# Performance work log

Measured on AMD Instinct MI355X. Metric: run time of the kernel, lower is better.

Reference implementation:

```python
import jax, jax.numpy as jnp
import numpy as np

T, B, L, CTX, H = 512, 512, 16, 64, 128
STATE_DIM, SHOT, PID, DATA = 32, 12, 35, 23


def setup_inputs() -> dict:
    key = jax.random.key(0)
    ks = jax.random.split(key, 64)
    k = iter(ks)
    def rn(shape, s=0.1):
        return (jax.random.normal(next(k), shape) * s).astype(jnp.float32)
    xs = jax.random.normal(next(k), (T, B, DATA), jnp.float32)
    xs = xs.at[:, :, 12].set(jax.random.randint(next(k), (T, B), 0, SHOT).astype(jnp.float32))
    xs = xs.at[:, :, 17].set(jax.random.randint(next(k), (T, B), 0, PID).astype(jnp.float32))
    xs = xs.at[:, :, 20].set(jax.random.randint(next(k), (T, B), 0, SHOT).astype(jnp.float32))
    return dict(
        total_xs=jnp.zeros((1,), jnp.float32),
        xs=xs,
        ts=jnp.linspace(0.0, 2.0, T).astype(jnp.float32),
        noise_std=jnp.asarray(0.1, jnp.float32),
        z0_noise=jax.random.normal(next(k), (B, L), jnp.float32),
        bm_noise=jax.random.normal(next(k), (T - 1, B, L), jnp.float32),
        shot_emb=rn((SHOT, 8)), player_emb=rn((PID, 8)),
        gru_wih=rn((3 * H, STATE_DIM)), gru_whh=rn((3 * H, H)),
        gru_bih=rn((3 * H,)), gru_bhh=rn((3 * H,)),
        enc_w=rn((CTX, H)), enc_b=rn((CTX,)),
        qz0_w=rn((2 * L, CTX)), qz0_b=rn((2 * L,)),
        f_w1=rn((H, L + CTX)), f_b1=rn((H,)), f_w2=rn((H, H)), f_b2=rn((H,)),
        f_w3=rn((L, H)), f_b3=rn((L,)),
        h_w1=rn((H, L)), h_b1=rn((H,)), h_w2=rn((H, H)), h_b2=rn((H,)),
        h_w3=rn((L, H)), h_b3=rn((L,)),
        g_w1=rn((L, H)), g_b1=rn((L, H)), g_w2=rn((L, H)), g_b2=rn((L,)),
        proj_w=rn((STATE_DIM, L)), proj_b=rn((STATE_DIM,)),
        pz0_mean=jnp.zeros((1, L), jnp.float32), pz0_logstd=jnp.zeros((1, L), jnp.float32),
        act_w=rn((128, L)), act_b=rn((128,)),
        act_land_w=rn((2, 128)), act_shot_w=rn((SHOT, 128)), act_move_w=rn((2, 128)),
    )


def _forward(xs, noise_std, shot_emb, player_emb, gru_wih, gru_whh, gru_bih, gru_bhh,
             enc_w, enc_b, qz0_w, qz0_b,
             f_w1, f_b1, f_w2, f_b2, f_w3, f_b3,
             h_w1, h_b1, h_w2, h_b2, h_w3, h_b3,
             g_w1, g_b1, g_w2, g_b2,
             proj_w, proj_b, pz0_mean, pz0_logstd,
             act_w, act_b, act_land_w, act_shot_w, act_move_w,
             ts, z0_noise, bm_noise):
    # --- SDE_embed_and_transform: replace shot/player id cols with embeddings ---
    state = xs[:, :, :18]
    shot_ids = state[:, :, 12].astype(jnp.int32)
    pid_ids = state[:, :, 17].astype(jnp.int32)
    state_t = jnp.concatenate([state[:, :, :12], shot_emb[shot_ids],
                               state[:, :, 13:17], player_emb[pid_ids]], axis=-1)  # (T,B,32)
    xs_t = jnp.concatenate([state_t, xs[:, :, 18:]], axis=-1)  # (T,B,37)
    # --- Encoder: GRU over time-reversed states, linear head, flip back ---
    def gru_step(h, xt):
        gi = xt @ gru_wih.T + gru_bih
        gh = h @ gru_whh.T + gru_bhh
        ir, iz, inn = jnp.split(gi, 3, axis=-1)
        hr, hz, hn = jnp.split(gh, 3, axis=-1)
        r = jax.nn.sigmoid(ir + hr)
        zg = jax.nn.sigmoid(iz + hz)
        n = jnp.tanh(inn + r * hn)
        hnew = (1.0 - zg) * n + zg * h
        return hnew, hnew
    h0 = jnp.zeros((xs.shape[1], gru_whh.shape[1]), xs.dtype)
    _, hs = jax.lax.scan(gru_step, h0, state_t[::-1])
    ctx = (hs @ enc_w.T + enc_b)[::-1]  # (T,B,CTX)
    # --- posterior z0 ---
    qm, qls = jnp.split(ctx[0] @ qz0_w.T + qz0_b, 2, axis=1)
    z0 = qm + jnp.exp(qls) * z0_noise
    # --- Euler-Maruyama with logqp; searchsorted(right) -> ctx[min(i+1,T-1)] = ctx[i+1] ---
    dts = ts[1:] - ts[:-1]  # (T-1,)
    dW = jnp.sqrt(dts)[:, None, None] * bm_noise
    ctx_steps = ctx[1:]
    def mlp3(x, w1, b1, w2, b2, w3, b3):
        h1 = jax.nn.softplus(x @ w1.T + b1)
        h2 = jax.nn.softplus(h1 @ w2.T + b2)
        return h2 @ w3.T + b3
    def g_diag(y):  # (B,L): per-latent-dim scalar nets, batched over L
        hg = jax.nn.softplus(y[:, :, None] * g_w1[None] + g_b1[None])  # (B,L,H)
        return jax.nn.sigmoid(jnp.einsum('blh,lh->bl', hg, g_w2) + g_b2)
    def sde_step(z, inp):
        c, dw, dt = inp
        f_val = mlp3(jnp.concatenate([z, c], axis=1), f_w1, f_b1, f_w2, f_b2, f_w3, f_b3)
        h_val = mlp3(z, h_w1, h_b1, h_w2, h_b2, h_w3, h_b3)
        g_val = g_diag(z)
        u = (f_val - h_val) / g_val
        logr = 0.5 * jnp.sum(u * u, axis=1) * dt
        z_new = z + f_val * dt + g_val * dw
        return z_new, (z_new, logr)
    _, (z_tail, log_ratio) = jax.lax.scan(sde_step, z0, (ctx_steps, dW, dts))
    zs = jnp.concatenate([z0[None], z_tail], axis=0)  # (T,B,L)
    _xs = zs @ proj_w.T + proj_b  # (T,B,32)
    # --- action model losses ---
    a = jax.nn.relu(zs @ act_w.T + act_b)
    land = (a @ act_land_w.T).reshape(-1, 2)
    shot_logits = (a @ act_shot_w.T).reshape(-1, act_shot_w.shape[0])
    move = (a @ act_move_w.T).reshape(-1, 2)
    true_actions = xs_t[:, :, -5:]
    true_land = true_actions[:, :, :2].reshape(-1, 2)
    true_move = true_actions[:, :, 3:].reshape(-1, 2)
    true_shot = true_actions[:, :, 2].astype(jnp.int32).reshape(-1)
    land_loss = jnp.mean((land - true_land) ** 2)
    move_loss = jnp.mean((move - true_move) ** 2)
    logp = jax.nn.log_softmax(shot_logits, axis=-1)
    picked = jnp.take_along_axis(logp, true_shot[:, None], axis=1)[:, 0]
    mask = (true_shot != 0).astype(logp.dtype)  # CrossEntropy ignore_index=0
    shot_loss = -jnp.sum(picked * mask) / jnp.maximum(jnp.sum(mask), 1.0)
    # --- reconstruction log-likelihood ---
    xs_state = xs_t[:, :, :STATE_DIM]
    LOG2PI = 1.8378770664093453
    log_pxs = jnp.mean(jnp.sum(
        -0.5 * ((xs_state - _xs) / noise_std) ** 2 - jnp.log(noise_std) - 0.5 * LOG2PI,
        axis=(0, 2)))
    # --- KL(q(z0) || p(z0)) ---
    var_q = jnp.exp(2.0 * qls)
    var_p = jnp.exp(2.0 * pz0_logstd)
    kl = pz0_logstd - qls + (var_q + (qm - pz0_mean) ** 2) / (2.0 * var_p) - 0.5
    logqp0 = jnp.mean(jnp.sum(kl, axis=1))
    logqp_path = jnp.mean(jnp.sum(log_ratio, axis=0))
    return log_pxs, logqp0 + logqp_path + land_loss + shot_loss + move_loss


def reference(total_xs, xs, ts, noise_std, z0_noise, bm_noise, shot_emb, player_emb,
              gru_wih, gru_whh, gru_bih, gru_bhh, enc_w, enc_b, qz0_w, qz0_b,
              f_w1, f_b1, f_w2, f_b2, f_w3, f_b3, h_w1, h_b1, h_w2, h_b2, h_w3, h_b3,
              g_w1, g_b1, g_w2, g_b2, proj_w, proj_b, pz0_mean, pz0_logstd,
              act_w, act_b, act_land_w, act_shot_w, act_move_w):
    return _forward(xs, noise_std, shot_emb, player_emb, gru_wih, gru_whh, gru_bih, gru_bhh,
                    enc_w, enc_b, qz0_w, qz0_b,
                    f_w1, f_b1, f_w2, f_b2, f_w3, f_b3,
                    h_w1, h_b1, h_w2, h_b2, h_w3, h_b3,
                    g_w1, g_b1, g_w2, g_b2,
                    proj_w, proj_b, pz0_mean, pz0_logstd,
                    act_w, act_b, act_land_w, act_shot_w, act_move_w,
                    ts, z0_noise, bm_noise)
```

## Files before the change

### kernel.cpp

```cpp
#include <hip/hip_runtime.h>
#include <cstdint>

typedef _Float16 f16;
typedef _Float16 f16x2 __attribute__((ext_vector_type(2)));

#define T_STEPS 512
#define B_SZ 512
#define LOG2PI 1.8378770664093453f

__device__ __forceinline__ uint32_t packh2(float a, float b) {
  f16x2 v; v[0] = (f16)a; v[1] = (f16)b;
  return __builtin_bit_cast(uint32_t, v);
}

__device__ __forceinline__ float fdot2(uint32_t a, uint32_t b, float c) {
#if defined(__AMDGCN__) && __has_builtin(__builtin_amdgcn_fdot2)
  return __builtin_amdgcn_fdot2(__builtin_bit_cast(f16x2, a),
                                __builtin_bit_cast(f16x2, b), c, false);
#else
  f16x2 x = __builtin_bit_cast(f16x2, a), y = __builtin_bit_cast(f16x2, b);
  return c + (float)x[0] * (float)y[0] + (float)x[1] * (float)y[1];
#endif
}

#define DOT4(acc, w0, w1, w2, w3, v)                                     \
  do {                                                                   \
    acc = fdot2((w0), (v).x, acc); acc = fdot2((w1), (v).y, acc);        \
    acc = fdot2((w2), (v).z, acc); acc = fdot2((w3), (v).w, acc);        \
  } while (0)

__device__ __forceinline__ float sigmoidf_(float x) {
  return 1.0f / (1.0f + __expf(-x));
}
__device__ __forceinline__ float tanhf_(float x) {
  float ax = fabsf(x);
  float t = __expf(-2.0f * ax);
  float r = (1.0f - t) / (1.0f + t);
  return copysignf(r, x);
}
__device__ __forceinline__ float softplusf_(float x) {
  return fmaxf(x, 0.0f) + __logf(1.0f + __expf(-fabsf(x)));
}

__global__ __launch_bounds__(256) void k_embed(
    const float* __restrict__ xs, const float* __restrict__ shot_emb,
    const float* __restrict__ player_emb, f16* __restrict__ state_t,
    float* __restrict__ accums) {
  if (blockIdx.x == 0 && threadIdx.x < 16) accums[threadIdx.x] = 0.0f;
  size_t idx = (size_t)blockIdx.x * 256 + threadIdx.x;
  const float* xp = xs + idx * 23;
  f16* op = state_t + idx * 32;
  int sid = (int)xp[12];
  int pid = (int)xp[17];
#pragma unroll
  for (int i = 0; i < 12; ++i) op[i] = (f16)xp[i];
  const float* se = shot_emb + sid * 8;
#pragma unroll
  for (int i = 0; i < 8; ++i) op[12 + i] = (f16)se[i];
#pragma unroll
  for (int i = 0; i < 4; ++i) op[20 + i] = (f16)xp[13 + i];
  const float* pe = player_emb + pid * 8;
#pragma unroll
  for (int i = 0; i < 8; ++i) op[24 + i] = (f16)pe[i];
}

__global__ __launch_bounds__(448, 4) void k_gru(
    const f16* __restrict__ state_t, const float* __restrict__ wih,
    const float* __restrict__ whh, const float* __restrict__ bih,
    const float* __restrict__ bhh, const float* __restrict__ enc_w,
    const float* __restrict__ enc_b, const float* __restrict__ qz0_w,
    const float* __restrict__ qz0_b, const float* __restrict__ z0_noise,
    const float* __restrict__ pz0_mean, const float* __restrict__ pz0_logstd,
    f16* __restrict__ ctx, float* __restrict__ z0_out,
    float* __restrict__ accums) {
  __shared__ __align__(16) uint32_t s_x[16];
  __shared__ __align__(16) uint32_t s_h[64];
  __shared__ float s_gi[384], s_gh[384];
  __shared__ float s_ctx0[64];
  __shared__ float s_q[32];

  const int tid = threadIdx.x;
  const int bg = blockIdx.x;
  const uint32_t* stu = (const uint32_t*)state_t;

  uint32_t wA[64];
  uint32_t wB[16];
  float bi = 0.f, bh = 0.f, encbr = 0.f;

  if (tid < 384) {
    const float* whr = whh + (size_t)tid * 128;
#pragma unroll
    for (int i = 0; i < 64; ++i) wA[i] = packh2(whr[2 * i], whr[2 * i + 1]);
    const float* wxr = wih + (size_t)tid * 32;
#pragma unroll
    for (int i = 0; i < 16; ++i) wB[i] = packh2(wxr[2 * i], wxr[2 * i + 1]);
    bi = bih[tid];
    bh = bhh[tid];
  } else {
    int cc = tid - 384;
    const float* wer = enc_w + (size_t)cc * 128;
#pragma unroll
    for (int i = 0; i < 64; ++i) wA[i] = packh2(wer[2 * i], wer[2 * i + 1]);
    encbr = enc_b[cc];
  }

  if (tid < 64) s_h[tid] = 0u;
  if (tid < 4)
    *(uint4*)&s_x[tid * 4] =
        *(const uint4*)(stu + ((size_t)(T_STEPS - 1) * B_SZ + bg) * 16 + tid * 4);
  float h_old = 0.0f;
  __syncthreads();

  for (int t = T_STEPS - 1; t >= 0; --t) {
    uint4 xpref = make_uint4(0, 0, 0, 0);
    if (tid >= 128 && tid < 132 && t > 0)
      xpref = *(const uint4*)(stu + ((size_t)(t - 1) * B_SZ + bg) * 16 +
                              (tid - 128) * 4);
    if (tid < 384) {
      float ax0 = bi, ax1 = 0.f;
      const uint4* xq = (const uint4*)s_x;
#pragma unroll
      for (int j = 0; j < 4; ++j) {
        uint4 v = xq[j];
        if (j & 1) { DOT4(ax1, wB[4 * j], wB[4 * j + 1], wB[4 * j + 2], wB[4 * j + 3], v); }
        else       { DOT4(ax0, wB[4 * j], wB[4 * j + 1], wB[4 * j + 2], wB[4 * j + 3], v); }
      }
      float ah0 = bh, ah1 = 0.f;
      const uint4* hq = (const uint4*)s_h;
#pragma unroll
      for (int j = 0; j < 16; ++j) {
        uint4 v = hq[j];
        if (j & 1) { DOT4(ah1, wA[4 * j], wA[4 * j + 1], wA[4 * j + 2], wA[4 * j + 3], v); }
        else       { DOT4(ah0, wA[4 * j], wA[4 * j + 1], wA[4 * j + 2], wA[4 * j + 3], v); }
      }
      s_gi[tid] = ax0 + ax1;
      s_gh[tid] = ah0 + ah1;
    } else if (t < T_STEPS - 1) {
      int cc = tid - 384;
      float a0 = encbr, a1 = 0.f;
      const uint4* hq = (const uint4*)s_h;
#pragma unroll
      for (int j = 0; j < 16; ++j) {
        uint4 v = hq[j];
        if (j & 1) { DOT4(a1, wA[4 * j], wA[4 * j + 1], wA[4 * j + 2], wA[4 * j + 3], v); }
        else       { DOT4(a0, wA[4 * j], wA[4 * j + 1], wA[4 * j + 2], wA[4 * j + 3], v); }
      }
      ctx[((size_t)(t + 1) * B_SZ + bg) * 64 + cc] = (f16)(a0 + a1);
    }
    __syncthreads();
    if (tid < 128) {
      float r = sigmoidf_(s_gi[tid] + s_gh[tid]);
      float zg = sigmoidf_(s_gi[128 + tid] + s_gh[128 + tid]);
      float n = tanhf_(s_gi[256 + tid] + r * s_gh[256 + tid]);
      float hnew = (1.0f - zg) * n + zg * h_old;
      h_old = hnew;
      ((f16*)s_h)[tid] = (f16)hnew;
    } else if (tid >= 128 && tid < 132 && t > 0) {
      *(uint4*)&s_x[(tid - 128) * 4] = xpref;
    }
    __syncthreads();
  }

  if (tid >= 384) {
    int cc = tid - 384;
    float a0 = encbr, a1 = 0.f;
    const uint4* hq = (const uint4*)s_h;
#pragma unroll
    for (int j = 0; j < 16; ++j) {
      uint4 v = hq[j];
      if (j & 1) { DOT4(a1, wA[4 * j], wA[4 * j + 1], wA[4 * j + 2], wA[4 * j + 3], v); }
      else       { DOT4(a0, wA[4 * j], wA[4 * j + 1], wA[4 * j + 2], wA[4 * j + 3], v); }
    }
    float val = a0 + a1;
    ctx[(size_t)bg * 64 + cc] = (f16)val;
    s_ctx0[cc] = val;
  }
  __syncthreads();
  if (tid < 32) {
    float acc = qz0_b[tid];
#pragma unroll 8
    for (int k = 0; k < 64; ++k) acc += qz0_w[tid * 64 + k] * s_ctx0[k];
    s_q[tid] = acc;
  }
  __syncthreads();
  if (tid < 16) {
    float qm = s_q[tid], qls = s_q[16 + tid];
    float z0v = qm + __expf(qls) * z0_noise[bg * 16 + tid];
    z0_out[bg * 16 + tid] = z0v;
    float pm = pz0_mean[tid], pls = pz0_logstd[tid];
    float var_q = __expf(2.0f * qls);
    float var_p = __expf(2.0f * pls);
    float dm = qm - pm;
    float kl = pls - qls + (var_q + dm * dm) / (2.0f * var_p) - 0.5f;
    atomicAdd(&accums[5], kl);
  }
}

__global__ __launch_bounds__(256, 2) void k_sde(
    const f16* __restrict__ ctx, const float* __restrict__ z0_in,
    const float* __restrict__ ts, const float* __restrict__ bm_noise,
    const float* __restrict__ fw1, const float* __restrict__ fb1,
    const float* __restrict__ fw2, const float* __restrict__ fb2,
    const float* __restrict__ fw3, const float* __restrict__ fb3,
    const float* __restrict__ hw1, const float* __restrict__ hb1,
    const float* __restrict__ hw2, const float* __restrict__ hb2,
    const float* __restrict__ hw3, const float* __restrict__ hb3,
    const float* __restrict__ gw1, const float* __restrict__ gb1,
    const float* __restrict__ gw2, const float* __restrict__ gb2,
    f16* __restrict__ zs, float* __restrict__ accums) {
  __shared__ __align__(16) uint32_t s_x2[40];
  __shared__ __align__(16) uint32_t s_h1f[64];
  __shared__ __align__(16) uint32_t s_h1h[64];
  __shared__ __align__(16) uint32_t s_h2[2][64];
  __shared__ float s_zf[16];
  __shared__ __align__(16) float s_gp[128];
  __shared__ __align__(16) float s_p3[256];
  __shared__ float s_dts[T_STEPS];

  const int tid = threadIdx.x;
  const int bg = blockIdx.x;

  uint32_t uw[56];
  uint32_t wP2[64];
  uint32_t wP3[8];
  float bias1r = 0.f, bias2r = 0.f, gb2r = 0.f, fb3r = 0.f, hb3r = 0.f;

  if (tid < 128) {
    const float* w = fw1 + (size_t)tid * 80;
#pragma unroll
    for (int i = 0; i < 40; ++i) uw[i] = packh2(w[2 * i], w[2 * i + 1]);
    bias1r = fb1[tid];
  } else {
    int u = tid - 128;
    const float* w = hw1 + (size_t)u * 16;
#pragma unroll
    for (int i = 0; i < 8; ++i) uw[i] = packh2(w[2 * i], w[2 * i + 1]);
    bias1r = hb1[u];
    int l = u & 15, k8 = u >> 4;
#pragma unroll
    for (int i = 0; i < 16; ++i) {
      int h = k8 * 16 + i;
      uw[8 + i] = __builtin_bit_cast(uint32_t, gw1[l * 128 + h]);
      uw[24 + i] = __builtin_bit_cast(uint32_t, gb1[l * 128 + h]);
      uw[40 + i] = __builtin_bit_cast(uint32_t, gw2[l * 128 + h]);
    }
  }
  {
    int mlp = tid >> 7, u = tid & 127;
    const float* w = (mlp ? hw2 : fw2) + (size_t)u * 128;
#pragma unroll
    for (int i = 0; i < 64; ++i) wP2[i] = packh2(w[2 * i], w[2 * i + 1]);
    bias2r = (mlp ? hb2 : fb2)[u];
  }
  {
    int mlp = tid >> 7, o = tid & 15, k8 = (tid >> 4) & 7;
    const float* w = (mlp ? hw3 : fw3) + (size_t)o * 128 + k8 * 16;
#pragma unroll
    for (int i = 0; i < 8; ++i) wP3[i] = packh2(w[2 * i], w[2 * i + 1]);
  }
  if (tid < 16) {
    fb3r = fb3[tid];
    hb3r = hb3[tid];
    gb2r = gb2[tid];
  }
  for (int i = tid; i < T_STEPS - 1; i += 256) s_dts[i] = ts[i + 1] - ts[i];

  if (tid < 16) {
    float z = z0_in[bg * 16 + tid];
    s_zf[tid] = z;
    ((f16*)s_x2)[tid] = (f16)z;
    zs[(size_t)bg * 16 + tid] = (f16)z;
  }
  if (tid >= 16 && tid < 24) {
    int q = tid - 16;
    *(uint4*)&s_x2[8 + q * 4] =
        *(const uint4*)((const uint32_t*)ctx + ((size_t)1 * B_SZ + bg) * 32 + q * 4);
  }
  float path_acc = 0.0f;
  __syncthreads();

  for (int t = 0; t < T_STEPS - 1; ++t) {
    float bm_cur = 0.f;
    uint4 cpref = make_uint4(0, 0, 0, 0);
    if (tid < 16) bm_cur = bm_noise[((size_t)t * B_SZ + bg) * 16 + tid];
    if (tid >= 16 && tid < 24 && t <= T_STEPS - 3) {
      int q = tid - 16;
      cpref = *(const uint4*)((const uint32_t*)ctx +
                              ((size_t)(t + 2) * B_SZ + bg) * 32 + q * 4);
    }
    if (tid < 128) {
      float a0 = bias1r, a1 = 0.f;
      const uint4* xq = (const uint4*)s_x2;
#pragma unroll
      for (int j = 0; j < 10; ++j) {
        uint4 v = xq[j];
        if (j & 1) { DOT4(a1, uw[4 * j], uw[4 * j + 1], uw[4 * j + 2], uw[4 * j + 3], v); }
        else       { DOT4(a0, uw[4 * j], uw[4 * j + 1], uw[4 * j + 2], uw[4 * j + 3], v); }
      }
      ((f16*)s_h1f)[tid] = (f16)softplusf_(a0 + a1);
    } else {
      int u = tid - 128;
      const uint4* zq = (const uint4*)s_x2;
      float a0 = bias1r, a1 = 0.f;
      uint4 v0 = zq[0], v1 = zq[1];
      DOT4(a0, uw[0], uw[1], uw[2], uw[3], v0);
      DOT4(a1, uw[4], uw[5], uw[6], uw[7], v1);
      ((f16*)s_h1h)[u] = (f16)softplusf_(a0 + a1);
      int l = u & 15, k8 = u >> 4;
      float y = s_zf[l];
      float acc = 0.f;
#pragma unroll
      for (int i = 0; i < 16; ++i) {
        float pre = fmaf(y, __builtin_bit_cast(float, uw[8 + i]),
                         __builtin_bit_cast(float, uw[24 + i]));
        acc = fmaf(softplusf_(pre), __builtin_bit_cast(float, uw[40 + i]), acc);
      }
      s_gp[l * 8 + k8] = acc;
    }
    __syncthreads();
    {
      const uint4* hq = (const uint4*)((tid >> 7) ? s_h1h : s_h1f);
      float a0 = bias2r, a1 = 0.f, a2 = 0.f, a3 = 0.f;
#pragma unroll
      for (int j = 0; j < 16; j += 4) {
        uint4 v0 = hq[j], v1 = hq[j + 1], v2 = hq[j + 2], v3 = hq[j + 3];
        DOT4(a0, wP2[4 * j], wP2[4 * j + 1], wP2[4 * j + 2], wP2[4 * j + 3], v0);
        DOT4(a1, wP2[4 * j + 4], wP2[4 * j + 5], wP2[4 * j + 6], wP2[4 * j + 7], v1);
        DOT4(a2, wP2[4 * j + 8], wP2[4 * j + 9], wP2[4 * j + 10], wP2[4 * j + 11], v2);
        DOT4(a3, wP2[4 * j + 12], wP2[4 * j + 13], wP2[4 * j + 14], wP2[4 * j + 15], v3);
      }
      ((f16*)s_h2[tid >> 7])[tid & 127] = (f16)softplusf_((a0 + a1) + (a2 + a3));
    }
    __syncthreads();
    {
      int mlp = tid >> 7, o = tid & 15, k8 = (tid >> 4) & 7;
      const uint4* hq = (const uint4*)&s_h2[mlp][k8 * 8];
      uint4 v0 = hq[0], v1 = hq[1];
      float a0 = 0.f, a1 = 0.f;
      DOT4(a0, wP3[0], wP3[1], wP3[2], wP3[3], v0);
      DOT4(a1, wP3[4], wP3[5], wP3[6], wP3[7], v1);
      s_p3[(mlp * 16 + o) * 8 + k8] = a0 + a1;
    }
    __syncthreads();
    if (tid < 16) {
      int l = tid;
      const float4* fp = (const float4*)&s_p3[l * 8];
      const float4* hp = (const float4*)&s_p3[(16 + l) * 8];
      const float4* gp = (const float4*)&s_gp[l * 8];
      float4 f0 = fp[0], f1v = fp[1], h0 = hp[0], h1v = hp[1];
      float4 g0 = gp[0], g1 = gp[1];
      float fv = fb3r + ((f0.x + f0.y) + (f0.z + f0.w)) +
                 ((f1v.x + f1v.y) + (f1v.z + f1v.w));
      float hv = hb3r + ((h0.x + h0.y) + (h0.z + h0.w)) +
                 ((h1v.x + h1v.y) + (h1v.z + h1v.w));
      float gv = sigmoidf_(gb2r + ((g0.x + g0.y) + (g0.z + g0.w)) +
                           ((g1.x + g1.y) + (g1.z + g1.w)));
      float dt = s_dts[t];
      float u = (fv - hv) / gv;
      float lsum = u * u;
      lsum += __shfl_xor(lsum, 1);
      lsum += __shfl_xor(lsum, 2);
      lsum += __shfl_xor(lsum, 4);
      lsum += __shfl_xor(lsum, 8);
      if (l == 0) path_acc += 0.5f * lsum * dt;
      float zn = s_zf[l] + fv * dt + gv * (sqrtf(dt) * bm_cur);
      s_zf[l] = zn;
      ((f16*)s_x2)[l] = (f16)zn;
      zs[((size_t)(t + 1) * B_SZ + bg) * 16 + l] = (f16)zn;
    } else if (tid >= 16 && tid < 24 && t <= T_STEPS - 3) {
      int q = tid - 16;
      *(uint4*)&s_x2[8 + q * 4] = cpref;
    }
    __syncthreads();
  }
  if (tid == 0) atomicAdd(&accums[6], path_acc);
}

__global__ __launch_bounds__(256) void k_dec(
    const f16* __restrict__ zs, const f16* __restrict__ state_t,
    const float* __restrict__ xs, const float* __restrict__ proj_w,
    const float* __restrict__ proj_b, const float* __restrict__ act_w,
    const float* __restrict__ act_b, const float* __restrict__ land_w,
    const float* __restrict__ shot_w, const float* __restrict__ move_w,
    float* __restrict__ accums) {
  __shared__ __align__(16) uint32_t s_proj[32 * 8];
  __shared__ __align__(16) uint32_t s_act[128 * 8];
  __shared__ __align__(16) uint32_t s_head[128 * 8];
  __shared__ float s_pb[32], s_ab[128];
  __shared__ float s_red[4 * 5];

  const int tid = threadIdx.x;
  if (tid < 256) {
    int i = tid >> 3, kp = tid & 7;
    s_proj[tid] = packh2(proj_w[i * 16 + 2 * kp], proj_w[i * 16 + 2 * kp + 1]);
  }
  for (int id = tid; id < 1024; id += 256) {
    int j = id >> 3, kp = id & 7;
    s_act[id] = packh2(act_w[j * 16 + 2 * kp], act_w[j * 16 + 2 * kp + 1]);
  }
  for (int id = tid; id < 1024; id += 256) {
    int j = id >> 3, p = id & 7;
    int h0 = 2 * p, h1 = 2 * p + 1;
    float w0 = (h0 < 2) ? land_w[h0 * 128 + j]
                        : (h0 < 14 ? shot_w[(h0 - 2) * 128 + j]
                                   : move_w[(h0 - 14) * 128 + j]);
    float w1 = (h1 < 2) ? land_w[h1 * 128 + j]
                        : (h1 < 14 ? shot_w[(h1 - 2) * 128 + j]
                                   : move_w[(h1 - 14) * 128 + j]);
    s_head[j * 8 + p] = packh2(w0, w1);
  }
  if (tid < 32) s_pb[tid] = proj_b[tid];
  if (tid < 128) s_ab[tid] = act_b[tid];
  __syncthreads();

  size_t idx0 = (size_t)blockIdx.x * 512 + tid;
  size_t idx1 = idx0 + 256;
  uint32_t zA[8], zB[8];
  {
    const uint4* za = (const uint4*)(zs + idx0 * 16);
    const uint4* zb = (const uint4*)(zs + idx1 * 16);
    uint4 a0 = za[0], a1 = za[1], b0 = zb[0], b1 = zb[1];
    zA[0] = a0.x; zA[1] = a0.y; zA[2] = a0.z; zA[3] = a0.w;
    zA[4] = a1.x; zA[5] = a1.y; zA[6] = a1.z; zA[7] = a1.w;
    zB[0] = b0.x; zB[1] = b0.y; zB[2] = b0.z; zB[3] = b0.w;
    zB[4] = b1.x; zB[5] = b1.y; zB[6] = b1.z; zB[7] = b1.w;
  }
  uint32_t stA[16], stB[16];
  {
// ... 118 lines not shown

extern "C" void kernel_launch(void* const* d_in, const int* in_sizes, int n_in,
                              void* d_out, int out_size, void* d_ws,
                              size_t ws_size, hipStream_t stream) {
  const float* xs = (const float*)d_in[1];
  const float* ts = (const float*)d_in[2];
  const float* noise_std = (const float*)d_in[3];
  const float* z0_noise = (const float*)d_in[4];
  const float* bm_noise = (const float*)d_in[5];
  const float* shot_emb = (const float*)d_in[6];
  const float* player_emb = (const float*)d_in[7];
  const float* gru_wih = (const float*)d_in[8];
  const float* gru_whh = (const float*)d_in[9];
  const float* gru_bih = (const float*)d_in[10];
  const float* gru_bhh = (const float*)d_in[11];
  const float* enc_w = (const float*)d_in[12];
  const float* enc_b = (const float*)d_in[13];
  const float* qz0_w = (const float*)d_in[14];
  const float* qz0_b = (const float*)d_in[15];
  const float* f_w1 = (const float*)d_in[16];
  const float* f_b1 = (const float*)d_in[17];
  const float* f_w2 = (const float*)d_in[18];
  const float* f_b2 = (const float*)d_in[19];
  const float* f_w3 = (const float*)d_in[20];
  const float* f_b3 = (const float*)d_in[21];
  const float* h_w1 = (const float*)d_in[22];
  const float* h_b1 = (const float*)d_in[23];
  const float* h_w2 = (const float*)d_in[24];
  const float* h_b2 = (const float*)d_in[25];
  const float* h_w3 = (const float*)d_in[26];
  const float* h_b3 = (const float*)d_in[27];
  const float* g_w1 = (const float*)d_in[28];
  const float* g_b1 = (const float*)d_in[29];
  const float* g_w2 = (const float*)d_in[30];
  const float* g_b2 = (const float*)d_in[31];
  const float* proj_w = (const float*)d_in[32];
  const float* proj_b = (const float*)d_in[33];
  const float* pz0_mean = (const float*)d_in[34];
  const float* pz0_logstd = (const float*)d_in[35];
  const float* act_w = (const float*)d_in[36];
  const float* act_b = (const float*)d_in[37];
  const float* act_land_w = (const float*)d_in[38];
  const float* act_shot_w = (const float*)d_in[39];
  const float* act_move_w = (const float*)d_in[40];

  char* ws = (char*)d_ws;
  float* accums = (float*)ws;
  f16* state_t = (f16*)(ws + 256);
  f16* ctx = (f16*)(ws + 256 + 16777216);
  float* z0b = (float*)(ws + 256 + 16777216 + 33554432);
  f16* zs = (f16*)(ws + 256 + 16777216 + 33554432 + 32768);

  k_embed<<<1024, 256, 0, stream>>>(xs, shot_emb, player_emb, state_t, accums);
  k_gru<<<512, 448, 0, stream>>>(state_t, gru_wih, gru_whh, gru_bih, gru_bhh,
                                 enc_w, enc_b, qz0_w, qz0_b, z0_noise, pz0_mean,
                                 pz0_logstd, ctx, z0b, accums);
  k_sde<<<512, 256, 0, stream>>>(ctx, z0b, ts, bm_noise, f_w1, f_b1, f_w2, f_b2,
                                 f_w3, f_b3, h_w1, h_b1, h_w2, h_b2, h_w3, h_b3,
                                 g_w1, g_b1, g_w2, g_b2, zs, accums);
  k_dec<<<512, 256, 0, stream>>>(zs, state_t, xs, proj_w, proj_b, act_w, act_b,
                                 act_land_w, act_shot_w, act_move_w, accums);
  k_fin<<<1, 64, 0, stream>>>(accums, noise_std, (float*)d_out);
}
```

Before: 2.005 ms.

## Repartition GRU and SDE recurrences so each thread computes two rows

The GRU kernel moves from 448 to 256 threads per block. Each thread now holds two gate rows and folds bih+bhh for the r/z gates, which drops one barrier-separated stage and lets the loop read x directly. Encoder context outputs are staged in a 64-row shared ring buffer and written to global memory in coalesced bursts. The SDE kernel is repartitioned the same way: two rows per thread, the final layer is reduced with shuffles instead of an extra shared-memory stage, and zs is buffered in shared memory and written once at the end. The intent is fewer barriers and less per-step global traffic, in exchange for much higher register pressure per thread and less thread-level parallelism per step.

```diff
diff --git a/kernel.cpp b/kernel.cpp
--- a/kernel.cpp
+++ b/kernel.cpp
@@ -64,7 +64,7 @@
   for (int i = 0; i < 8; ++i) op[24 + i] = (f16)pe[i];
 }
 
-__global__ __launch_bounds__(448, 4) void k_gru(
+__global__ __launch_bounds__(256, 2) void k_gru(
     const f16* __restrict__ state_t, const float* __restrict__ wih,
     const float* __restrict__ whh, const float* __restrict__ bih,
     const float* __restrict__ bhh, const float* __restrict__ enc_w,
@@ -73,9 +73,10 @@
     const float* __restrict__ pz0_mean, const float* __restrict__ pz0_logstd,
     f16* __restrict__ ctx, float* __restrict__ z0_out,
     float* __restrict__ accums) {
-  __shared__ __align__(16) uint32_t s_x[16];
   __shared__ __align__(16) uint32_t s_h[64];
-  __shared__ float s_gi[384], s_gh[384];
+  __shared__ __align__(16) float s_grz[128][2];
+  __shared__ __align__(16) float s_gn[128][2];
+  __shared__ __align__(16) f16 s_cbuf[64][64];
   __shared__ float s_ctx0[64];
   __shared__ float s_q[32];
 
@@ -83,100 +84,176 @@
   const int bg = blockIdx.x;
   const uint32_t* stu = (const uint32_t*)state_t;
 
-  uint32_t wA[64];
-  uint32_t wB[16];
-  float bi = 0.f, bh = 0.f, encbr = 0.f;
-
-  if (tid < 384) {
-    const float* whr = whh + (size_t)tid * 128;
-#pragma unroll
-    for (int i = 0; i < 64; ++i) wA[i] = packh2(whr[2 * i], whr[2 * i + 1]);
-    const float* wxr = wih + (size_t)tid * 32;
-#pragma unroll
-    for (int i = 0; i < 16; ++i) wB[i] = packh2(wxr[2 * i], wxr[2 * i + 1]);
-    bi = bih[tid];
-    bh = bhh[tid];
+  uint32_t wh0[64], wh1[64], wx0[16], wx1[16];
+  float b0 = 0.f, b1 = 0.f, b0h = 0.f, b1h = 0.f, encbr = 0.f;
+
+  if (tid < 128) {
+    const float* r0 = whh + (size_t)tid * 128;
+    const float* r1 = whh + (size_t)(128 + tid) * 128;
+#pragma unroll
+    for (int i = 0; i < 64; ++i) {
+      wh0[i] = packh2(r0[2 * i], r0[2 * i + 1]);
+      wh1[i] = packh2(r1[2 * i], r1[2 * i + 1]);
+    }
+    const float* x0 = wih + (size_t)tid * 32;
+    const float* x1 = wih + (size_t)(128 + tid) * 32;
+#pragma unroll
+    for (int i = 0; i < 16; ++i) {
+      wx0[i] = packh2(x0[2 * i], x0[2 * i + 1]);
+      wx1[i] = packh2(x1[2 * i], x1[2 * i + 1]);
+    }
+    b0 = bih[tid] + bhh[tid];
+    b1 = bih[128 + tid] + bhh[128 + tid];
+  } else if (tid < 192) {
+    int u = tid - 128;
+    const float* r0 = whh + (size_t)(256 + 2 * u) * 128;
+    const float* r1 = whh + (size_t)(256 + 2 * u + 1) * 128;
+#pragma unroll
+    for (int i = 0; i < 64; ++i) {
+      wh0[i] = packh2(r0[2 * i], r0[2 * i + 1]);
+      wh1[i] = packh2(r1[2 * i], r1[2 * i + 1]);
+    }
+    const float* x0 = wih + (size_t)(256 + 2 * u) * 32;
+    const float* x1 = wih + (size_t)(256 + 2 * u + 1) * 32;
+#pragma unroll
+    for (int i = 0; i < 16; ++i) {
+      wx0[i] = packh2(x0[2 * i], x0[2 * i + 1]);
+      wx1[i] = packh2(x1[2 * i], x1[2 * i + 1]);
+    }
+    b0 = bih[256 + 2 * u];
+    b0h = bhh[256 + 2 * u];
+    b1 = bih[256 + 2 * u + 1];
+    b1h = bhh[256 + 2 * u + 1];
   } else {
-    int cc = tid - 384;
-    const float* wer = enc_w + (size_t)cc * 128;
-#pragma unroll
-    for (int i = 0; i < 64; ++i) wA[i] = packh2(wer[2 * i], wer[2 * i + 1]);
-    encbr = enc_b[cc];
+    int c = tid - 192;
+    const float* er = enc_w + (size_t)c * 128;
+#pragma unroll
+    for (int i = 0; i < 64; ++i) wh0[i] = packh2(er[2 * i], er[2 * i + 1]);
+    encbr = enc_b[c];
   }
 
   if (tid < 64) s_h[tid] = 0u;
-  if (tid < 4)
-    *(uint4*)&s_x[tid * 4] =
-        *(const uint4*)(stu + ((size_t)(T_STEPS - 1) * B_SZ + bg) * 16 + tid * 4);
   float h_old = 0.0f;
   __syncthreads();
 
   for (int t = T_STEPS - 1; t >= 0; --t) {
-    uint4 xpref = make_uint4(0, 0, 0, 0);
-    if (tid >= 128 && tid < 132 && t > 0)
-      xpref = *(const uint4*)(stu + ((size_t)(t - 1) * B_SZ + bg) * 16 +
-                              (tid - 128) * 4);
-    if (tid < 384) {
-      float ax0 = bi, ax1 = 0.f;
-      const uint4* xq = (const uint4*)s_x;
-#pragma unroll
-      for (int j = 0; j < 4; ++j) {
-        uint4 v = xq[j];
-        if (j & 1) { DOT4(ax1, wB[4 * j], wB[4 * j + 1], wB[4 * j + 2], wB[4 * j + 3], v); }
-        else       { DOT4(ax0, wB[4 * j], wB[4 * j + 1], wB[4 * j + 2], wB[4 * j + 3], v); }
-      }
-      float ah0 = bh, ah1 = 0.f;
+    const uint4* xr = (const uint4*)(stu + ((size_t)t * B_SZ + bg) * 16);
+    uint4 xv0 = xr[0], xv1 = xr[1], xv2 = xr[2], xv3 = xr[3];
+    if (tid < 128) {
+      float aR = b0, aRb = 0.f, aZ = b1, aZb = 0.f;
+      DOT4(aR, wx0[0], wx0[1], wx0[2], wx0[3], xv0);
+      DOT4(aRb, wx0[4], wx0[5], wx0[6], wx0[7], xv1);
+      DOT4(aR, wx0[8], wx0[9], wx0[10], wx0[11], xv2);
+      DOT4(aRb, wx0[12], wx0[13], wx0[14], wx0[15], xv3);
+      DOT4(aZ, wx1[0], wx1[1], wx1[2], wx1[3], xv0);
+      DOT4(aZb, wx1[4], wx1[5], wx1[6], wx1[7], xv1);
+      DOT4(aZ, wx1[8], wx1[9], wx1[10], wx1[11], xv2);
+      DOT4(aZb, wx1[12], wx1[13], wx1[14], wx1[15], xv3);
       const uint4* hq = (const uint4*)s_h;
 #pragma unroll
       for (int j = 0; j < 16; ++j) {
         uint4 v = hq[j];
-        if (j & 1) { DOT4(ah1, wA[4 * j], wA[4 * j + 1], wA[4 * j + 2], wA[4 * j + 3], v); }
-        else       { DOT4(ah0, wA[4 * j], wA[4 * j + 1], wA[4 * j + 2], wA[4 * j + 3], v); }
+        if (j & 1) {
+          DOT4(aRb, wh0[4 * j], wh0[4 * j + 1], wh0[4 * j + 2], wh0[4 * j + 3], v);
+          DOT4(aZb, wh1[4 * j], wh1[4 * j + 1], wh1[4 * j + 2], wh1[4 * j + 3], v);
+        } else {
+          DOT4(aR, wh0[4 * j], wh0[4 * j + 1], wh0[4 * j + 2], wh0[4 * j + 3], v);
+          DOT4(aZ, wh1[4 * j], wh1[4 * j + 1], wh1[4 * j + 2], wh1[4 * j + 3], v);
+        }
       }
-      s_gi[tid] = ax0 + ax1;
-      s_gh[tid] = ah0 + ah1;
-    } else if (t < T_STEPS - 1) {
-      int cc = tid - 384;
-      float a0 = encbr, a1 = 0.f;
+      *(float2*)&s_grz[tid][0] = make_float2(aR + aRb, aZ + aZb);
+    } else if (tid < 192) {
+      int u = tid - 128;
+      float aI0 = b0, aI0b = 0.f, aI1 = b1, aI1b = 0.f;
+      DOT4(aI0, wx0[0], wx0[1], wx0[2], wx0[3], xv0);
+      DOT4(aI0b, wx0[4], wx0[5], wx0[6], wx0[7], xv1);
+      DOT4(aI0, wx0[8], wx0[9], wx0[10], wx0[11], xv2);
+      DOT4(aI0b, wx0[12], wx0[13], wx0[14], wx0[15], xv3);
+      DOT4(aI1, wx1[0], wx1[1], wx1[2], wx1[3], xv0);
+      DOT4(aI1b, wx1[4], wx1[5], wx1[6], wx1[7], xv1);
+      DOT4(aI1, wx1[8], wx1[9], wx1[10], wx1[11], xv2);
+      DOT4(aI1b, wx1[12], wx1[13], wx1[14], wx1[15], xv3);
+      float aH0 = b0h, aH0b = 0.f, aH1 = b1h, aH1b = 0.f;
       const uint4* hq = (const uint4*)s_h;
 #pragma unroll
       for (int j = 0; j < 16; ++j) {
         uint4 v = hq[j];
-        if (j & 1) { DOT4(a1, wA[4 * j], wA[4 * j + 1], wA[4 * j + 2], wA[4 * j + 3], v); }
-        else       { DOT4(a0, wA[4 * j], wA[4 * j + 1], wA[4 * j + 2], wA[4 * j + 3], v); }
+        if (j & 1) {
+          DOT4(aH0b, wh0[4 * j], wh0[4 * j + 1], wh0[4 * j + 2], wh0[4 * j + 3], v);
+          DOT4(aH1b, wh1[4 * j], wh1[4 * j + 1], wh1[4 * j + 2], wh1[4 * j + 3], v);
+        } else {
+          DOT4(aH0, wh0[4 * j], wh0[4 * j + 1], wh0[4 * j + 2], wh0[4 * j + 3], v);
+          DOT4(aH1, wh1[4 * j], wh1[4 * j + 1], wh1[4 * j + 2], wh1[4 * j + 3], v);
+        }
       }
-      ctx[((size_t)(t + 1) * B_SZ + bg) * 64 + cc] = (f16)(a0 + a1);
+      *(float4*)&s_gn[2 * u][0] =
+          make_float4(aI0 + aI0b, aH0 + aH0b, aI1 + aI1b, aH1 + aH1b);
+    } else if (t < T_STEPS - 1) {
+      int c = tid - 192;
+      float e0 = encbr, e1 = 0.f;
+      const uint4* hq = (const uint4*)s_h;
+#pragma unroll
+      for (int j = 0; j < 16; ++j) {
+        uint4 v = hq[j];
+        if (j & 1) {
+          DOT4(e1, wh0[4 * j], wh0[4 * j + 1], wh0[4 * j + 2], wh0[4 * j + 3], v);
+        } else {
+          DOT4(e0, wh0[4 * j], wh0[4 * j + 1], wh0[4 * j + 2], wh0[4 * j + 3], v);
+        }
+      }
+      s_cbuf[(t + 1) & 63][c] = (f16)(e0 + e1);
     }
     __syncthreads();
     if (tid < 128) {
-      float r = sigmoidf_(s_gi[tid] + s_gh[tid]);
-      float zg = sigmoidf_(s_gi[128 + tid] + s_gh[128 + tid]);
-      float n = tanhf_(s_gi[256 + tid] + r * s_gh[256 + tid]);
+      float2 rz = *(const float2*)&s_grz[tid][0];
+      float2 nn = *(const float2*)&s_gn[tid][0];
+      float r = sigmoidf_(rz.x);
+      float zg = sigmoidf_(rz.y);
+      float n = tanhf_(nn.x + r * nn.y);
       float hnew = (1.0f - zg) * n + zg * h_old;
       h_old = hnew;
       ((f16*)s_h)[tid] = (f16)hnew;
-    } else if (tid >= 128 && tid < 132 && t > 0) {
-      *(uint4*)&s_x[(tid - 128) * 4] = xpref;
+    } else if (tid >= 192 && (t & 63) == 63) {
+      int lane = tid & 63;
+      int seg = lane & 7;
+#pragma unroll
+      for (int it = 0; it < 8; ++it) {
+        int row = (t + 1) + it * 8 + (lane >> 3);
+        uint4 v = *(const uint4*)((const uint32_t*)&s_cbuf[row & 63][0] + seg * 4);
+        *(uint4*)((uint32_t*)ctx + ((size_t)row * B_SZ + bg) * 32 + seg * 4) = v;
+      }
     }
     __syncthreads();
   }
 
-  if (tid >= 384) {
-    int cc = tid - 384;
-    float a0 = encbr, a1 = 0.f;
+  if (tid >= 192) {
+    int c = tid - 192;
+    float e0 = encbr, e1 = 0.f;
     const uint4* hq = (const uint4*)s_h;
 #pragma unroll
     for (int j = 0; j < 16; ++j) {
       uint4 v = hq[j];
-      if (j & 1) { DOT4(a1, wA[4 * j], wA[4 * j + 1], wA[4 * j + 2], wA[4 * j + 3], v); }
-      else       { DOT4(a0, wA[4 * j], wA[4 * j + 1], wA[4 * j + 2], wA[4 * j + 3], v); }
-    }
-    float val = a0 + a1;
-    ctx[(size_t)bg * 64 + cc] = (f16)val;
-    s_ctx0[cc] = val;
+      if (j & 1) {
+        DOT4(e1, wh0[4 * j], wh0[4 * j + 1], wh0[4 * j + 2], wh0[4 * j + 3], v);
+      } else {
+        DOT4(e0, wh0[4 * j], wh0[4 * j + 1], wh0[4 * j + 2], wh0[4 * j + 3], v);
+      }
+    }
+    float val = e0 + e1;
+    s_ctx0[c] = val;
+    s_cbuf[0][c] = (f16)val;
   }
   __syncthreads();
-  if (tid < 32) {
+  if (tid >= 192) {
+    int lane = tid & 63;
+    int seg = lane & 7;
+#pragma unroll
+    for (int it = 0; it < 8; ++it) {
+      int row = it * 8 + (lane >> 3);
+      uint4 v = *(const uint4*)((const uint32_t*)&s_cbuf[row][0] + seg * 4);
+      *(uint4*)((uint32_t*)ctx + ((size_t)row * B_SZ + bg) * 32 + seg * 4) = v;
+    }
+  } else if (tid < 32) {
     float acc = qz0_b[tid];
 #pragma unroll 8
     for (int k = 0; k < 64; ++k) acc += qz0_w[tid * 64 + k] * s_ctx0[k];
@@ -208,172 +285,254 @@
     const float* __restrict__ gw1, const float* __restrict__ gb1,
     const float* __restrict__ gw2, const float* __restrict__ gb2,
     f16* __restrict__ zs, float* __restrict__ accums) {
-  __shared__ __align__(16) uint32_t s_x2[40];
+  __shared__ __align__(16) uint32_t s_x2z[8];
+  __shared__ float s_zf[16];
   __shared__ __align__(16) uint32_t s_h1f[64];
   __shared__ __align__(16) uint32_t s_h1h[64];
   __shared__ __align__(16) uint32_t s_h2[2][64];
-  __shared__ float s_zf[16];
-  __shared__ __align__(16) float s_gp[128];
-  __shared__ __align__(16) float s_p3[256];
+  __shared__ float s_gpw[2][16];
+  __shared__ __align__(16) float s_v3[32];
   __shared__ float s_dts[T_STEPS];
+  __shared__ __align__(16) f16 s_zbuf[T_STEPS * 16];
 
   const int tid = threadIdx.x;
   const int bg = blockIdx.x;
 
-  uint32_t uw[56];
-  uint32_t wP2[64];
-  uint32_t wP3[8];
-  float bias1r = 0.f, bias2r = 0.f, gb2r = 0.f, fb3r = 0.f, hb3r = 0.f;
-
-  if (tid < 128) {
-    const float* w = fw1 + (size_t)tid * 80;
-#pragma unroll
-    for (int i = 0; i < 40; ++i) uw[i] = packh2(w[2 * i], w[2 * i + 1]);
-    bias1r = fb1[tid];
+  uint32_t wa[80];
+  uint32_t wb[32];
+  float gw1v[16], gb1v[16], gw2v[16];
+  float ba = 0.f, bb = 0.f, fb3r = 0.f, hb3r = 0.f, gb2r = 0.f;
+
+  if (tid < 64) {
+    const float* r0 = fw1 + (size_t)(2 * tid) * 80;
+    const float* r1 = fw1 + (size_t)(2 * tid + 1) * 80;
+#pragma unroll
+    for (int i = 0; i < 40; ++i) {
+      wa[i] = packh2(r0[2 * i], r0[2 * i + 1]);
+      wa[40 + i] = packh2(r1[2 * i], r1[2 * i + 1]);
+    }
+    ba = fb1[2 * tid];
+    bb = fb1[2 * tid + 1];
+    int k8 = tid >> 3, mlp = (tid >> 2) & 1, o4 = tid & 3;
+    const float* w3src = mlp ? hw3 : fw3;
+#pragma unroll
+    for (int oo = 0; oo < 4; ++oo)
+#pragma unroll
+      for (int j = 0; j < 8; ++j)
+        wb[oo * 8 + j] = packh2(w3src[(o4 * 4 + oo) * 128 + k8 * 16 + 2 * j],
+                                w3src[(o4 * 4 + oo) * 128 + k8 * 16 + 2 * j + 1]);
+    if (tid < 16) {
+      fb3r = fb3[tid];
+      hb3r = hb3[tid];
+      gb2r = gb2[tid];
+    }
+  } else if (tid < 128) {
+    int u = tid - 64;
+    const float* r0 = fw2 + (size_t)(2 * u) * 128;
+    const float* r1 = fw2 + (size_t)(2 * u + 1) * 128;
+#pragma unroll
+    for (int i = 0; i < 64; ++i) {
+      wa[i] = packh2(r0[2 * i], r0[2 * i + 1]);
+      wb[i & 15] = wb[i & 15];
+    }
+    ba = fb2[2 * u];
+    bb = fb2[2 * u + 1];
+    int l = u & 15, c4 = u >> 4;
+#pragma unroll
+    for (int j = 0; j < 16; ++j) {
+      int h = c4 * 16 + j;
+      gw1v[j] = gw1[l * 128 + h];
+      gb1v[j] = gb1[l * 128 + h];
+      gw2v[j] = gw2[l * 128 + h];
+    }
+  } else if (tid < 192) {
+    int u = tid - 128;
+    const float* r0 = hw2 + (size_t)(2 * u) * 128;
+#pragma unroll
+    for (int i = 0; i < 64; ++i) wa[i] = packh2(r0[2 * i], r0[2 * i + 1]);
+    const float* z0r = hw1 + (size_t)(2 * u) * 16;
+    const float* z1r = hw1 + (size_t)(2 * u + 1) * 16;
+#pragma unroll
+    for (int i = 0; i < 8; ++i) {
+      wb[i] = packh2(z0r[2 * i], z0r[2 * i + 1]);
+      wb[8 + i] = packh2(z1r[2 * i], z1r[2 * i + 1]);
+    }
+    ba = hb2[2 * u];
+    bb = hb2[2 * u + 1];
   } else {
+    int i2 = tid - 192;
+    int l = i2 & 15, c4 = i2 >> 4;
+#pragma unroll
+    for (int j = 0; j < 16; ++j) {
+      int h = 64 + c4 * 16 + j;
+      gw1v[j] = gw1[l * 128 + h];
+      gb1v[j] = gb1[l * 128 + h];
+      gw2v[j] = gw2[l * 128 + h];
+    }
+  }
+  uint32_t wc[64];
+  if (tid >= 64 && tid < 128) {
+    int u = tid - 64;
+    const float* r1 = fw2 + (size_t)(2 * u + 1) * 128;
+#pragma unroll
+    for (int i = 0; i < 64; ++i) wc[i] = packh2(r1[2 * i], r1[2 * i + 1]);
+  } else if (tid >= 128 && tid < 192) {
     int u = tid - 128;
-    const float* w = hw1 + (size_t)u * 16;
-#pragma unroll
-    for (int i = 0; i < 8; ++i) uw[i] = packh2(w[2 * i], w[2 * i + 1]);
-    bias1r = hb1[u];
-    int l = u & 15, k8 = u >> 4;
-#pragma unroll
-    for (int i = 0; i < 16; ++i) {
-      int h = k8 * 16 + i;
-      uw[8 + i] = __builtin_bit_cast(uint32_t, gw1[l * 128 + h]);
-      uw[24 + i] = __builtin_bit_cast(uint32_t, gb1[l * 128 + h]);
-      uw[40 + i] = __builtin_bit_cast(uint32_t, gw2[l * 128 + h]);
-    }
-  }
-  {
-    int mlp = tid >> 7, u = tid & 127;
-    const float* w = (mlp ? hw2 : fw2) + (size_t)u * 128;
-#pragma unroll
-    for (int i = 0; i < 64; ++i) wP2[i] = packh2(w[2 * i], w[2 * i + 1]);
-    bias2r = (mlp ? hb2 : fb2)[u];
-  }
-  {
-    int mlp = tid >> 7, o = tid & 15, k8 = (tid >> 4) & 7;
-    const float* w = (mlp ? hw3 : fw3) + (size_t)o * 128 + k8 * 16;
-#pragma unroll
-    for (int i = 0; i < 8; ++i) wP3[i] = packh2(w[2 * i], w[2 * i + 1]);
-  }
+    const float* r1 = hw2 + (size_t)(2 * u + 1) * 128;
+#pragma unroll
+    for (int i = 0; i < 64; ++i) wc[i] = packh2(r1[2 * i], r1[2 * i + 1]);
+  }
+  float hb1a = 0.f, hb1b = 0.f;
+  if (tid >= 128 && tid < 192) {
+    int u = tid - 128;
+    hb1a = hb1[2 * u];
+    hb1b = hb1[2 * u + 1];
+  }
+
+  for (int i = tid; i < T_STEPS - 1; i += 256) s_dts[i] = ts[i + 1] - ts[i];
+  float zf_r = 0.f;
   if (tid < 16) {
-    fb3r = fb3[tid];
-    hb3r = hb3[tid];
-    gb2r = gb2[tid];
-  }
-  for (int i = tid; i < T_STEPS - 1; i += 256) s_dts[i] = ts[i + 1] - ts[i];
-
-  if (tid < 16) {
-    float z = z0_in[bg * 16 + tid];
-    s_zf[tid] = z;
-    ((f16*)s_x2)[tid] = (f16)z;
-    zs[(size_t)bg * 16 + tid] = (f16)z;
-  }
-  if (tid >= 16 && tid < 24) {
-    int q = tid - 16;
-    *(uint4*)&s_x2[8 + q * 4] =
-        *(const uint4*)((const uint32_t*)ctx + ((size_t)1 * B_SZ + bg) * 32 + q * 4);
+    zf_r = z0_in[bg * 16 + tid];
+    s_zf[tid] = zf_r;
+    s_zbuf[tid] = (f16)zf_r;
+  }
+  if (tid < 8) {
+    float za = z0_in[bg * 16 + 2 * tid], zb = z0_in[bg * 16 + 2 * tid + 1];
+    s_x2z[tid] = packh2(za, zb);
   }
   float path_acc = 0.0f;
   __syncthreads();
 
   for (int t = 0; t < T_STEPS - 1; ++t) {
     float bm_cur = 0.f;
-    uint4 cpref = make_uint4(0, 0, 0, 0);
     if (tid < 16) bm_cur = bm_noise[((size_t)t * B_SZ + bg) * 16 + tid];
-    if (tid >= 16 && tid < 24 && t <= T_STEPS - 3) {
-      int q = tid - 16;
-      cpref = *(const uint4*)((const uint32_t*)ctx +
-                              ((size_t)(t + 2) * B_SZ + bg) * 32 + q * 4);
-    }
-    if (tid < 128) {
-      float a0 = bias1r, a1 = 0.f;
-      const uint4* xq = (const uint4*)s_x2;
-#pragma unroll
-      for (int j = 0; j < 10; ++j) {
-        uint4 v = xq[j];
-        if (j & 1) { DOT4(a1, uw[4 * j], uw[4 * j + 1], uw[4 * j + 2], uw[4 * j + 3], v); }
-        else       { DOT4(a0, uw[4 * j], uw[4 * j + 1], uw[4 * j + 2], uw[4 * j + 3], v); }
-      }
-      ((f16*)s_h1f)[tid] = (f16)softplusf_(a0 + a1);
-    } else {
-      int u = tid - 128;
-      const uint4* zq = (const uint4*)s_x2;
-      float a0 = bias1r, a1 = 0.f;
-      uint4 v0 = zq[0], v1 = zq[1];
-      DOT4(a0, uw[0], uw[1], uw[2], uw[3], v0);
-      DOT4(a1, uw[4], uw[5], uw[6], uw[7], v1);
-      ((f16*)s_h1h)[u] = (f16)softplusf_(a0 + a1);
-      int l = u & 15, k8 = u >> 4;
+    if (tid < 64) {
+      const uint4* cr =
+          (const uint4*)((const uint32_t*)ctx + ((size_t)(t + 1) * B_SZ + bg) * 32);
+      uint4 c0 = cr[0], c1 = cr[1], c2 = cr[2], c3 = cr[3];
+      uint4 c4v = cr[4], c5 = cr[5], c6 = cr[6], c7 = cr[7];
+      const uint4* zq = (const uint4*)s_x2z;
+      uint4 zv0 = zq[0], zv1 = zq[1];
+      float a0 = ba, a0b = 0.f, a1 = bb, a1b = 0.f;
+      DOT4(a0, wa[0], wa[1], wa[2], wa[3], zv0);
+      DOT4(a0b, wa[4], wa[5], wa[6], wa[7], zv1);
+      DOT4(a1, wa[40], wa[41], wa[42], wa[43], zv0);
+      DOT4(a1b, wa[44], wa[45], wa[46], wa[47], zv1);
+      DOT4(a0, wa[8], wa[9], wa[10], wa[11], c0);
+      DOT4(a0b, wa[12], wa[13], wa[14], wa[15], c1);
+      DOT4(a0, wa[16], wa[17], wa[18], wa[19], c2);
+      DOT4(a0b, wa[20], wa[21], wa[22], wa[23], c3);
+      DOT4(a0, wa[24], wa[25], wa[26], wa[27], c4v);
+      DOT4(a0b, wa[28], wa[29], wa[30], wa[31], c5);
+      DOT4(a0, wa[32], wa[33], wa[34], wa[35], c6);
+      DOT4(a0b, wa[36], wa[37], wa[38], wa[39], c7);
+      DOT4(a1, wa[48], wa[49], wa[50], wa[51], c0);
+      DOT4(a1b, wa[52], wa[53], wa[54], wa[55], c1);
+      DOT4(a1, wa[56], wa[57], wa[58], wa[59], c2);
+      DOT4(a1b, wa[60], wa[61], wa[62], wa[63], c3);
+      DOT4(a1, wa[64], wa[65], wa[66], wa[67], c4v);
+      DOT4(a1b, wa[68], wa[69], wa[70], wa[71], c5);
+      DOT4(a1, wa[72], wa[73], wa[74], wa[75], c6);
+      DOT4(a1b, wa[76], wa[77], wa[78], wa[79], c7);
+      s_h1f[tid] = packh2(softplusf_(a0 + a0b), softplusf_(a1 + a1b));
+    } else if (tid < 128 || tid >= 192) {
+      int i2 = (tid < 128) ? (tid - 64) : (tid - 192);
+      int half = (tid < 128) ? 0 : 1;
+      int l = i2 & 15;
       float y = s_zf[l];
       float acc = 0.f;
 #pragma unroll
-      for (int i = 0; i < 16; ++i) {
-        float pre = fmaf(y, __builtin_bit_cast(float, uw[8 + i]),
-                         __builtin_bit_cast(float, uw[24 + i]));
-        acc = fmaf(softplusf_(pre), __builtin_bit_cast(float, uw[40 + i]), acc);
+      for (int j = 0; j < 16; ++j) {
+        float pre = fmaf(y, gw1v[j], gb1v[j]);
+        acc = fmaf(softplusf_(pre), gw2v[j], acc);
       }
-      s_gp[l * 8 + k8] = acc;
+      acc += __shfl_xor(acc, 16);
+      acc += __shfl_xor(acc, 32);
+      if ((i2 & 63) < 16) s_gpw[half][l] = acc;
+      if (half) goto a_done;
+a_done:;
+    }
+    if (tid >= 128 && tid < 192) {
+      int u = tid - 128;
+      const uint4* zq = (const uint4*)s_x2z;
+      uint4 zv0 = zq[0], zv1 = zq[1];
+      float a0 = hb1a, a0b = 0.f, a1 = hb1b, a1b = 0.f;
+      DOT4(a0, wb[0], wb[1], wb[2], wb[3], zv0);
+      DOT4(a0b, wb[4], wb[5], wb[6], wb[7], zv1);
+      DOT4(a1, wb[8], wb[9], wb[10], wb[11], zv0);
+      DOT4(a1b, wb[12], wb[13], wb[14], wb[15], zv1);
+      s_h1h[u] = packh2(softplusf_(a0 + a0b), softplusf_(a1 + a1b));
     }
     __syncthreads();
-    {
-      const uint4* hq = (const uint4*)((tid >> 7) ? s_h1h : s_h1f);
-      float a0 = bias2r, a1 = 0.f, a2 = 0.f, a3 = 0.f;
-#pragma unroll
-      for (int j = 0; j < 16; j += 4) {
-        uint4 v0 = hq[j], v1 = hq[j + 1], v2 = hq[j + 2], v3 = hq[j + 3];
-        DOT4(a0, wP2[4 * j], wP2[4 * j + 1], wP2[4 * j + 2], wP2[4 * j + 3], v0);
-        DOT4(a1, wP2[4 * j + 4], wP2[4 * j + 5], wP2[4 * j + 6], wP2[4 * j + 7], v1);
-        DOT4(a2, wP2[4 * j + 8], wP2[4 * j + 9], wP2[4 * j + 10], wP2[4 * j + 11], v2);
-        DOT4(a3, wP2[4 * j + 12], wP2[4 * j + 13], wP2[4 * j + 14], wP2[4 * j + 15], v3);
+    if (tid >= 64 && tid < 192) {
+      int isH = tid >= 128;
+      int u = isH ? (tid - 128) : (tid - 64);
+      const uint4* hq = (const uint4*)(isH ? s_h1h : s_h1f);
+      float a0 = ba, a0b = 0.f, a1 = bb, a1b = 0.f;
+#pragma unroll
+      for (int j = 0; j < 16; ++j) {
+        uint4 v = hq[j];
+        if (j & 1) {
+          DOT4(a0b, wa[4 * j], wa[4 * j + 1], wa[4 * j + 2], wa[4 * j + 3], v);
+          DOT4(a1b, wc[4 * j], wc[4 * j + 1], wc[4 * j + 2], wc[4 * j + 3], v);
+        } else {
+          DOT4(a0, wa[4 * j], wa[4 * j + 1], wa[4 * j + 2], wa[4 * j + 3], v);
+          DOT4(a1, wc[4 * j], wc[4 * j + 1], wc[4 * j + 2], wc[4 * j + 3], v);
+        }
       }
-      ((f16*)s_h2[tid >> 7])[tid & 127] = (f16)softplusf_((a0 + a1) + (a2 + a3));
+      s_h2[isH][u] = packh2(softplusf_(a0 + a0b), softplusf_(a1 + a1b));
     }
     __syncthreads();
-    {
-      int mlp = tid >> 7, o = tid & 15, k8 = (tid >> 4) & 7;
+    if (tid < 64) {
+      int k8 = tid >> 3, mlp = (tid >> 2) & 1, o4 = tid & 3;
       const uint4* hq = (const uint4*)&s_h2[mlp][k8 * 8];
-      uint4 v0 = hq[0], v1 = hq[1];
-      float a0 = 0.f, a1 = 0.f;
-      DOT4(a0, wP3[0], wP3[1], wP3[2], wP3[3], v0);
-      DOT4(a1, wP3[4], wP3[5], wP3[6], wP3[7], v1);
-      s_p3[(mlp * 16 + o) * 8 + k8] = a0 + a1;
-    }
-    __syncthreads();
-    if (tid < 16) {
-      int l = tid;
-      const float4* fp = (const float4*)&s_p3[l * 8];
-      const float4* hp = (const float4*)&s_p3[(16 + l) * 8];
-      const float4* gp = (const float4*)&s_gp[l * 8];
-      float4 f0 = fp[0], f1v = fp[1], h0 = hp[0], h1v = hp[1];
-      float4 g0 = gp[0], g1 = gp[1];
-      float fv = fb3r + ((f0.x + f0.y) + (f0.z + f0.w)) +
-                 ((f1v.x + f1v.y) + (f1v.z + f1v.w));
-      float hv = hb3r + ((h0.x + h0.y) + (h0.z + h0.w)) +
-                 ((h1v.x + h1v.y) + (h1v.z + h1v.w));
-      float gv = sigmoidf_(gb2r + ((g0.x + g0.y) + (g0.z + g0.w)) +
-                           ((g1.x + g1.y) + (g1.z + g1.w)));
+      uint4 hv0 = hq[0], hv1 = hq[1];
+      float a0 = 0.f, a1 = 0.f, a2 = 0.f, a3 = 0.f;
+      DOT4(a0, wb[0], wb[1], wb[2], wb[3], hv0);
+      DOT4(a0, wb[4], wb[5], wb[6], wb[7], hv1);
+      DOT4(a1, wb[8], wb[9], wb[10], wb[11], hv0);
+      DOT4(a1, wb[12], wb[13], wb[14], wb[15], hv1);
+      DOT4(a2, wb[16], wb[17], wb[18], wb[19], hv0);
+      DOT4(a2, wb[20], wb[21], wb[22], wb[23], hv1);
+      DOT4(a3, wb[24], wb[25], wb[26], wb[27], hv0);
+      DOT4(a3, wb[28], wb[29], wb[30], wb[31], hv1);
+      a0 += __shfl_xor(a0, 8); a0 += __shfl_xor(a0, 16); a0 += __shfl_xor(a0, 32);
+      a1 += __shfl_xor(a1, 8); a1 += __shfl_xor(a1, 16); a1 += __shfl_xor(a1, 32);
+      a2 += __shfl_xor(a2, 8); a2 += __shfl_xor(a2, 16); a2 += __shfl_xor(a2, 32);
+      a3 += __shfl_xor(a3, 8); a3 += __shfl_xor(a3, 16); a3 += __shfl_xor(a3, 32);
+      if (tid < 8)
+        *(float4*)&s_v3[mlp * 16 + o4 * 4] = make_float4(a0, a1, a2, a3);
+      int l = tid & 15;
+      float fv = s_v3[l] + fb3r;
+      float hv = s_v3[16 + l] + hb3r;
+      float gv = sigmoidf_(gb2r + s_gpw[0][l] + s_gpw[1][l]);
       float dt = s_dts[t];
-      float u = (fv - hv) / gv;
-      float lsum = u * u;
+      float uu = (fv - hv) / gv;
+      float lsum = uu * uu;
       lsum += __shfl_xor(lsum, 1);
       lsum += __shfl_xor(lsum, 2);
       lsum += __shfl_xor(lsum, 4);
       lsum += __shfl_xor(lsum, 8);
-      if (l == 0) path_acc += 0.5f * lsum * dt;
-      float zn = s_zf[l] + fv * dt + gv * (sqrtf(dt) * bm_cur);
-      s_zf[l] = zn;
-      ((f16*)s_x2)[l] = (f16)zn;
-      zs[((size_t)(t + 1) * B_SZ + bg) * 16 + l] = (f16)zn;
-    } else if (tid >= 16 && tid < 24 && t <= T_STEPS - 3) {
-      int q = tid - 16;
-      *(uint4*)&s_x2[8 + q * 4] = cpref;
+      if (tid == 0) path_acc += 0.5f * lsum * dt;
+      float zn = zf_r + fv * dt + gv * (sqrtf(dt) * bm_cur);
+      float zo = __shfl_xor(zn, 1);
+      if (tid < 16) {
+        zf_r = zn;
+        s_zf[tid] = zn;
+        s_zbuf[(t + 1) * 16 + tid] = (f16)zn;
+        if (!(tid & 1)) s_x2z[tid >> 1] = packh2(zn, zo);
+      }
     }
     __syncthreads();
   }
   if (tid == 0) atomicAdd(&accums[6], path_acc);
+#pragma unroll
+  for (int it = 0; it < 4; ++it) {
+    int idx = it * 256 + tid;
+    int row = idx >> 1, half = idx & 1;
+    uint4 v = *(const uint4*)((const uint32_t*)s_zbuf + row * 8 + half * 4);
+    *(uint4*)((uint32_t*)zs + ((size_t)row * B_SZ + bg) * 8 + half * 4) = v;
+  }
 }
 
 __global__ __launch_bounds__(256) void k_dec(
@@ -598,7 +757,7 @@
   f16* zs = (f16*)(ws + 256 + 16777216 + 33554432 + 32768);
 
   k_embed<<<1024, 256, 0, stream>>>(xs, shot_emb, player_emb, state_t, accums);
-  k_gru<<<512, 448, 0, stream>>>(state_t, gru_wih, gru_whh, gru_bih, gru_bhh,
+  k_gru<<<512, 256, 0, stream>>>(state_t, gru_wih, gru_whh, gru_bih, gru_bhh,
                                  enc_w, enc_b, qz0_w, qz0_b, z0_noise, pz0_mean,
                                  pz0_logstd, ctx, z0b, accums);
   k_sde<<<512, 256, 0, stream>>>(ctx, z0b, ts, bm_noise, f_w1, f_b1, f_w2, f_b2,
```

New measurement: 2.981 ms. 1.49x slower.
